# Kernel tuning notes

Hardware: AMD Instinct MI355X
Metric: run time of the kernel (lower is better)

The kernel has to match this reference:

```python
import jax, jax.numpy as jnp
import numpy as np

B, S, T = 16, 128, 128
E, H, D = 512, 512, 1024      # emb, encoder hidden, decoder hidden
VIN, VOUT = 10000, 10000


def setup_inputs() -> dict:
    key = jax.random.key(0)
    ks = iter(jax.random.split(key, 32))
    def w(shape, s=0.02):
        return jax.random.normal(next(ks), shape, jnp.float32) * s
    return {
        "x": jax.random.randint(next(ks), (B, S), 0, VIN),
        "gs_output": jax.random.randint(next(ks), (B, T), 0, VOUT),
        "in_emb": w((VIN, E)),
        "out_emb": w((VOUT, E)),
        "enc_wih0": w((2, 4 * H, E)), "enc_whh0": w((2, 4 * H, H)), "enc_b0": w((2, 4 * H)),
        "enc_wih1": w((2, 4 * H, 2 * H)), "enc_whh1": w((2, 4 * H, H)), "enc_b1": w((2, 4 * H)),
        "dec_wih0": w((4 * D, 2 * H + E)), "dec_whh0": w((4 * D, D)), "dec_b0": w((4 * D,)),
        "dec_wih1": w((4 * D, D)), "dec_whh1": w((4 * D, D)), "dec_b1": w((4 * D,)),
        "attn_w": w((D, 2 * H + D)), "attn_b": w((D,)),
        "attn_v": jax.random.uniform(next(ks), (D,), jnp.float32),
        "out_w": w((VOUT, D)), "out_b": w((VOUT,)),
    }


def _lstm_cell(x, h, c, wih, whh, b):
    # PyTorch gate order: i, f, g, o
    g = x @ wih.T + h @ whh.T + b
    i, f, gg, o = jnp.split(g, 4, axis=-1)
    c = jax.nn.sigmoid(f) * c + jax.nn.sigmoid(i) * jnp.tanh(gg)
    h = jax.nn.sigmoid(o) * jnp.tanh(c)
    return h, c


def _lstm_scan(xs, wih, whh, b, reverse=False):
    # xs: [T, B, in] time-major; returns hidden states [T, B, H]
    Bn, Hh = xs.shape[1], whh.shape[1]
    z = jnp.zeros((Bn, Hh), xs.dtype)
    def step(carry, x):
        h, c = _lstm_cell(x, carry[0], carry[1], wih, whh, b)
        return (h, c), h
    _, hs = jax.lax.scan(step, (z, z), xs, reverse=reverse)
    return hs


def reference(x, gs_output, in_emb, out_emb,
              enc_wih0, enc_whh0, enc_b0, enc_wih1, enc_whh1, enc_b1,
              dec_wih0, dec_whh0, dec_b0, dec_wih1, dec_whh1, dec_b1,
              attn_w, attn_b, attn_v, out_w, out_b):
    # padding_idx=0 rows are zero (matches nn.Embedding(padding_idx=0))
    in_emb = in_emb.at[0].set(0.0)
    out_emb = out_emb.at[0].set(0.0)
    Bn, Sn = x.shape

    # ---- bidirectional 2-layer encoder (eval mode, dropout off) ----
    xs = in_emb[x].transpose(1, 0, 2)  # [S, B, E]
    l0 = jnp.concatenate([
        _lstm_scan(xs, enc_wih0[0], enc_whh0[0], enc_b0[0]),
        _lstm_scan(xs, enc_wih0[1], enc_whh0[1], enc_b0[1], reverse=True)], -1)
    enc = jnp.concatenate([
        _lstm_scan(l0, enc_wih1[0], enc_whh1[0], enc_b1[0]),
        _lstm_scan(l0, enc_wih1[1], enc_whh1[1], enc_b1[1], reverse=True)], -1)
    enc_out = enc.transpose(1, 0, 2)  # [B, S, 2H]

    dec_layers = ((dec_wih0, dec_whh0, dec_b0), (dec_wih1, dec_whh1, dec_b1))

    def dec_step(h, c, inp):
        hs, cs = [], []
        for l, (wih, whh, b) in enumerate(dec_layers):
            nh, nc = _lstm_cell(inp, h[l], c[l], wih, whh, b)
            hs.append(nh); cs.append(nc); inp = nh
        return jnp.stack(hs), jnp.stack(cs), inp

    # torch primes decoder_hidden with one zero-input step from zero state
    h = jnp.zeros((2, Bn, D), jnp.float32)
    c = jnp.zeros((2, Bn, D), jnp.float32)
    h, c, _ = dec_step(h, c, jnp.zeros((Bn, 2 * H + E), jnp.float32))

    gs_emb = out_emb[gs_output].transpose(1, 0, 2)  # [T, B, E]

    def step(carry, emb_t):
        h, c, last_emb = carry
        q = c[-1]  # torch uses decoder_hidden[-1][-1] = last-layer CELL state
        qrep = jnp.broadcast_to(q[:, None, :], (Bn, Sn, D))
        energy = jnp.tanh(jnp.einsum('bsk,dk->bsd', jnp.concatenate([qrep, enc_out], -1), attn_w) + attn_b)
        a = jax.nn.softmax(energy @ attn_v, axis=1)           # [B, S]
        weighted = jnp.einsum('bs,bsh->bh', a, enc_out)       # [B, 2H]
        h2, c2, top = dec_step(h, c, jnp.concatenate([weighted, last_emb], -1))
        logits = top @ out_w.T + out_b                        # [B, Vout]
        return (h2, c2, emb_t), logits

    init = (h, c, jnp.zeros((Bn, E), jnp.float32))
    _, outs = jax.lax.scan(step, init, gs_emb)                # [T, B, Vout]
    return outs.transpose(1, 0, 2)                            # [B, T, Vout]
```

## Files before the change

### kernel.cpp

```cpp
#include <hip/hip_runtime.h>

#define BB 16
#define SS 128
#define TT 128
#define EE 512
#define HH 512
#define DD 1024
#define VO 10000

typedef _Float16 half4_t __attribute__((ext_vector_type(4)));
typedef _Float16 half8_t __attribute__((ext_vector_type(8)));

#define FMA4(A, W, X)              \
  A = fmaf((W).x, (X).x, A);       \
  A = fmaf((W).y, (X).y, A);       \
  A = fmaf((W).z, (X).z, A);       \
  A = fmaf((W).w, (X).w, A)

__device__ __forceinline__ float4 h2f4(half4_t h) {
  return make_float4((float)h[0], (float)h[1], (float)h[2], (float)h[3]);
}

__device__ __forceinline__ float wred(float s) {
#pragma unroll
  for (int off = 32; off >= 1; off >>= 1) s += __shfl_xor(s, off, 64);
  return s;
}
__device__ __forceinline__ float sigm(float x) { return 1.f / (1.f + expf(-x)); }

__device__ __forceinline__ void stv(float* p, float v) {
  __hip_atomic_store(p, v, __ATOMIC_RELAXED, __HIP_MEMORY_SCOPE_AGENT);
}

__device__ __forceinline__ void gbar2(unsigned* bar, int lb, int nblk, unsigned target) {
  asm volatile("s_waitcnt vmcnt(0) lgkmcnt(0)" ::: "memory");
  __syncthreads();
  if (threadIdx.x == 0)
    __hip_atomic_store(bar + lb * 16, target, __ATOMIC_RELAXED, __HIP_MEMORY_SCOPE_AGENT);
  if (lb == 0) {
    for (int i = threadIdx.x; i < nblk; i += blockDim.x)
      while (__hip_atomic_load(bar + i * 16, __ATOMIC_RELAXED, __HIP_MEMORY_SCOPE_AGENT) <
             target)
        __builtin_amdgcn_s_sleep(1);
    __syncthreads();
    if (threadIdx.x == 0)
      __hip_atomic_store(bar + 8192, target, __ATOMIC_RELAXED, __HIP_MEMORY_SCOPE_AGENT);
  }
  if (threadIdx.x == 0)
    while (__hip_atomic_load(bar + 8192, __ATOMIC_RELAXED, __HIP_MEMORY_SCOPE_AGENT) <
           target)
      __builtin_amdgcn_s_sleep(1);
  __syncthreads();
}

__global__ void f2h_k(const float* __restrict__ src, _Float16* __restrict__ dst, int n8) {
  const int i = blockIdx.x * blockDim.x + threadIdx.x;
  if (i < n8) {
    const float4 a = *(const float4*)&src[i * 8];
    const float4 b = *(const float4*)&src[i * 8 + 4];
    half8_t h;
    h[0] = a.x; h[1] = a.y; h[2] = a.z; h[3] = a.w;
    h[4] = b.x; h[5] = b.y; h[6] = b.z; h[7] = b.w;
    *(half8_t*)&dst[i * 8] = h;
  }
}

__global__ void gather_k(const int* __restrict__ idx, const float* __restrict__ emb,
                         float* __restrict__ out, int Sn) {
  const int s = blockIdx.x, b = blockIdx.y, tid = threadIdx.x;
  const int id = idx[b * Sn + s];
  float4 v = make_float4(0.f, 0.f, 0.f, 0.f);
  if (id != 0) v = ((const float4*)(emb + (size_t)id * EE))[tid];
  ((float4*)(out + ((size_t)s * BB + b) * EE))[tid] = v;
}

template <int K>
__global__ void gemv16b_k(const float* __restrict__ X, int ldx,
                          const float* __restrict__ W, int ldw,
                          float* __restrict__ G, int M, size_t wz, size_t gz) {
  const int lane = threadIdx.x & 63;
  const int n = blockIdx.x * 4 + (threadIdx.x >> 6);
  const int mg = blockIdx.y;
  const int z = blockIdx.z;
  const float* Xr = X + (size_t)mg * 16 * ldx;
  const float* Wn = W + (size_t)z * wz + (size_t)n * ldw;
  float acc[16];
#pragma unroll
  for (int j = 0; j < 16; ++j) acc[j] = 0.f;
#pragma unroll
  for (int it = 0; it < K / 256; ++it) {
    const int k = it * 256 + lane * 4;
    const float4 w4 = *(const float4*)&Wn[k];
#pragma unroll
    for (int j = 0; j < 16; ++j) {
      const float4 xv = *(const float4*)&Xr[(size_t)j * ldx + k];
      FMA4(acc[j], w4, xv);
    }
  }
#pragma unroll
  for (int j = 0; j < 16; ++j) acc[j] = wred(acc[j]);
  float sel = 0.f;
#pragma unroll
  for (int j = 0; j < 16; ++j)
    if (lane == j) sel = acc[j];
  if (lane < 16) G[(size_t)z * gz + (size_t)n * M + mg * 16 + lane] = sel;
}

__global__ __launch_bounds__(512, 4) void enc_mega7_k(
    const float* __restrict__ gx, const float* __restrict__ whh,
    const float* __restrict__ bias, float* __restrict__ h_all,
    float* __restrict__ seq, int seq_ts, int seq_bs, unsigned* __restrict__ barbase) {
  const int tid = threadIdx.x, lane = tid & 63, lw = tid >> 6;
  const int dir = blockIdx.x >> 7;
  const int lb = blockIdx.x & 127;
  const int w2 = lb * 8 + lw;
  const int d = w2 >> 1, bq = w2 & 1;
  unsigned* bar = barbase + dir * 16384;

  __shared__ float hs[16][512];

  float wr[4][8];
  const float* wsrc = whh + (size_t)dir * (4 * HH * HH);
#pragma unroll
  for (int g = 0; g < 4; ++g)
#pragma unroll
    for (int j = 0; j < 8; ++j)
      wr[g][j] = wsrc[(size_t)(g * HH + d) * HH + j * 64 + lane];
  float bv[4];
#pragma unroll
  for (int g = 0; g < 4; ++g) bv[g] = bias[dir * 4 * HH + g * HH + d];
  const float* gxz = gx + (size_t)dir * ((size_t)4 * HH * 2048);
  float creg = 0.f;
  unsigned bt = 0;

  for (int t = 0; t < SS; ++t) {
    const int idx = dir ? (SS - 1 - t) : t;
    const float* hp = h_all + ((size_t)t * 2 + dir) * (BB * HH);
    for (int i = tid; i < BB * HH / 4; i += 512)
      *(float4*)&((float*)hs)[i * 4] = *(const float4*)&hp[i * 4];
    __syncthreads();
    float acc[4][8];
#pragma unroll
    for (int g = 0; g < 4; ++g)
#pragma unroll
      for (int j = 0; j < 8; ++j) acc[g][j] = 0.f;
#pragma unroll
    for (int kb = 0; kb < 8; ++kb) {
      const int k = kb * 64 + lane;
#pragma unroll
      for (int j = 0; j < 8; ++j) {
        const float xv = hs[bq * 8 + j][k];
#pragma unroll
        for (int g = 0; g < 4; ++g) acc[g][j] = fmaf(wr[g][kb], xv, acc[g][j]);
      }
    }
#pragma unroll
    for (int g = 0; g < 4; ++g)
#pragma unroll
      for (int j = 0; j < 8; ++j) acc[g][j] = wred(acc[g][j]);
    float s0 = 0.f, s1 = 0.f, s2 = 0.f, s3 = 0.f;
#pragma unroll
    for (int j = 0; j < 8; ++j)
      if (lane == j) { s0 = acc[0][j]; s1 = acc[1][j]; s2 = acc[2][j]; s3 = acc[3][j]; }
    if (lane < 8) {
      const int b = bq * 8 + lane;
      const int m = idx * 16 + b;
      const float gi = sigm(s0 + bv[0] + gxz[(size_t)(0 * HH + d) * 2048 + m]);
      const float gf = sigm(s1 + bv[1] + gxz[(size_t)(1 * HH + d) * 2048 + m]);
      const float gg = tanhf(s2 + bv[2] + gxz[(size_t)(2 * HH + d) * 2048 + m]);
      const float go = sigm(s3 + bv[3] + gxz[(size_t)(3 * HH + d) * 2048 + m]);
      const float cn = gf * creg + gi * gg;
      creg = cn;
      const float hv = go * tanhf(cn);
      stv(h_all + ((size_t)(t + 1) * 2 + dir) * (BB * HH) + b * HH + d, hv);
      seq[(size_t)idx * seq_ts + (size_t)b * seq_bs + dir * HH + d] = hv;
    }
    gbar2(bar, lb, 128, ++bt);
  }
}

__global__ __launch_bounds__(1024, 4) void dec_mega7h_k(
    const float* __restrict__ gs_emb, const float* __restrict__ encWe,
    const float* __restrict__ enc_out, const _Float16* __restrict__ aw16,
    const float* __restrict__ attn_b, const float* __restrict__ attn_v,
    const _Float16* __restrict__ w16i0, const _Float16* __restrict__ w16h0,
    const float* __restrict__ b0, const _Float16* __restrict__ w16i1,
    const _Float16* __restrict__ w16h1, const float* __restrict__ b1,
    const float* __restrict__ zeros, float* __restrict__ h0_all,
    float* __restrict__ h1_all, float* __restrict__ c1_all, float* __restrict__ wtd_all,
    float* __restrict__ qW_all, float* __restrict__ scores_all,
    unsigned* __restrict__ bar) {
  const int tid = threadIdx.x, lane = tid & 63, lw = tid >> 6;
  const int blk = blockIdx.x;
  const int w = blk * 16 + lw;
  const int d = w >> 2, bq = w & 3;
  const int b_att = blk >> 4, shard = blk & 15;

  __shared__ float xch[4][4][16];
  __shared__ float sco[SS];
  __shared__ float sred[16][64];

  const _Float16* w0i0 = w16i0 + (size_t)(0 * DD + d) * 1536;
  const _Float16* w0i1 = w16i0 + (size_t)(1 * DD + d) * 1536;
  const _Float16* w0i2 = w16i0 + (size_t)(2 * DD + d) * 1536;
  const _Float16* w0i3 = w16i0 + (size_t)(3 * DD + d) * 1536;
  const _Float16* w0h0 = w16h0 + (size_t)(0 * DD + d) * 1024;
  const _Float16* w0h1 = w16h0 + (size_t)(1 * DD + d) * 1024;
  const _Float16* w0h2 = w16h0 + (size_t)(2 * DD + d) * 1024;
  const _Float16* w0h3 = w16h0 + (size_t)(3 * DD + d) * 1024;
  const _Float16* w1i0 = w16i1 + (size_t)(0 * DD + d) * 1024;
  const _Float16* w1i1 = w16i1 + (size_t)(1 * DD + d) * 1024;
  const _Float16* w1i2 = w16i1 + (size_t)(2 * DD + d) * 1024;
  const _Float16* w1i3 = w16i1 + (size_t)(3 * DD + d) * 1024;
  const _Float16* w1h0 = w16h1 + (size_t)(0 * DD + d) * 1024;
  const _Float16* w1h1 = w16h1 + (size_t)(1 * DD + d) * 1024;
  const _Float16* w1h2 = w16h1 + (size_t)(2 * DD + d) * 1024;
  const _Float16* w1h3 = w16h1 + (size_t)(3 * DD + d) * 1024;
  float bv0[4], bv1[4];
#pragma unroll
  for (int g = 0; g < 4; ++g) { bv0[g] = b0[g * DD + d]; bv1[g] = b1[g * DD + d]; }
  const float abv = attn_b[d];
  float c0 = 0.f, c1 = 0.f;
  unsigned bt = 0;

  if (lw == ((d & 3) << 2) && lane < 16) {
  }
  if (bq == 0 && lane < 16) {
  }
  if (bq == 0 && lane < 16) {
    const float cn = sigm(bv0[0]) * tanhf(bv0[2]);
    c0 = cn;
    stv(h0_all + lane * DD + d, sigm(bv0[3]) * tanhf(cn));
  }
  gbar2(bar, blk, 256, ++bt);
  {
    float acc[4][4];
#pragma unroll
    for (int g = 0; g < 4; ++g)
#pragma unroll
      for (int j = 0; j < 4; ++j) acc[g][j] = 0.f;
#pragma unroll
    for (int it = 0; it < 4; ++it) {
      const int k = it * 256 + lane * 4;
      const float4 q0 = h2f4(*(const half4_t*)&w1i0[k]);
      const float4 q1 = h2f4(*(const half4_t*)&w1i1[k]);
      const float4 q2 = h2f4(*(const half4_t*)&w1i2[k]);
      const float4 q3 = h2f4(*(const half4_t*)&w1i3[k]);
#pragma unroll
      for (int j = 0; j < 4; ++j) {
        const float4 xv = *(const float4*)&h0_all[(bq * 4 + j) * DD + k];
        FMA4(acc[0][j], q0, xv);
        FMA4(acc[1][j], q1, xv);
        FMA4(acc[2][j], q2, xv);
        FMA4(acc[3][j], q3, xv);
      }
    }
#pragma unroll
    for (int g = 0; g < 4; ++g)
#pragma unroll
      for (int j = 0; j < 4; ++j) acc[g][j] = wred(acc[g][j]);
    float s[4] = {0.f, 0.f, 0.f, 0.f};
#pragma unroll
    for (int j = 0; j < 4; ++j)
      if (lane == j) { s[0] = acc[0][j]; s[1] = acc[1][j]; s[2] = acc[2][j]; s[3] = acc[3][j]; }
    if (lane < 4) {
      const int b = bq * 4 + lane;
      const float cn = sigm(s[0] + bv1[0]) * tanhf(s[2] + bv1[2]);
      c1 = cn;
      stv(c1_all + b * DD + d, cn);
      stv(h1_all + b * DD + d, sigm(s[3] + bv1[3]) * tanhf(cn));
    }
  }
  gbar2(bar, blk, 256, ++bt);

  for (int t = 0; t < TT; ++t) {
    {
      const float* cb = c1_all + (size_t)t * (BB * DD);
      float qa[4] = {0.f, 0.f, 0.f, 0.f};
#pragma unroll
      for (int it = 0; it < 4; ++it) {
        const int k = it * 256 + lane * 4;
        const float4 w4 = h2f4(*(const half4_t*)&aw16[(size_t)d * 2048 + k]);
#pragma unroll
        for (int j = 0; j < 4; ++j) {
          const float4 xv = *(const float4*)&cb[(bq * 4 + j) * DD + k];
          FMA4(qa[j], w4, xv);
        }
      }
#pragma unroll
      for (int j = 0; j < 4; ++j) qa[j] = wred(qa[j]);
      float sel = 0.f;
#pragma unroll
      for (int j = 0; j < 4; ++j)
        if (lane == j) sel = qa[j];
      if (lane < 4)
        stv(qW_all + (size_t)t * (BB * DD) + (bq * 4 + lane) * DD + d, sel + abv);
    }
    gbar2(bar, blk, 256, ++bt);
    if (lw < 8) {
      const int s = shard * 8 + lw;
      const float* ew = encWe + ((size_t)(b_att * SS + s)) * DD;
      const float* qb = qW_all + (size_t)t * (BB * DD) + b_att * DD;
      float a = 0.f;
#pragma unroll
      for (int it = 0; it < 4; ++it) {
        const int k = it * 256 + lane * 4;
        const float4 e4 = *(const float4*)&ew[k];
        const float4 q4 = *(const float4*)&qb[k];
        const float4 v4 = *(const float4*)&attn_v[k];
        a += v4.x * tanhf(q4.x + e4.x) + v4.y * tanhf(q4.y + e4.y) +
             v4.z * tanhf(q4.z + e4.z) + v4.w * tanhf(q4.w + e4.w);
      }
      a = wred(a);
      if (lane == 0) stv(scores_all + (size_t)t * (BB * SS) + b_att * SS + s, a);
    }
    gbar2(bar, blk, 256, ++bt);
    {
      if (tid < SS) sco[tid] = scores_all[(size_t)t * (BB * SS) + b_att * SS + tid];
      __syncthreads();
      float m = -1e30f;
      for (int s = 0; s < SS; ++s) m = fmaxf(m, sco[s]);
      __syncthreads();
      if (tid < SS) sco[tid] = expf(sco[tid] - m);
      __syncthreads();
      float sum = 0.f;
      for (int s = 0; s < SS; ++s) sum += sco[s];
      const float inv = 1.f / sum;
      float p = 0.f;
#pragma unroll
      for (int i = 0; i < 8; ++i) {
        const int s = lw * 8 + i;
        p += sco[s] * enc_out[((size_t)(b_att * SS + s)) * DD + shard * 64 + lane];
      }
      sred[lw][lane] = p;
      __syncthreads();
      if (lw == 0) {
        float a2 = 0.f;
#pragma unroll
        for (int i = 0; i < 16; ++i) a2 += sred[i][lane];
        stv(wtd_all + (size_t)t * (BB * DD) + b_att * DD + shard * 64 + lane, a2 * inv);
      }
    }
    gbar2(bar, blk, 256, ++bt);
    {
      const float* xw = wtd_all + (size_t)t * (BB * DD);
      const float* em = t ? gs_emb + (size_t)(t - 1) * (BB * EE) : zeros;
      const float* hp = h0_all + (size_t)t * (BB * DD);
      float acc[4][4];
#pragma unroll
      for (int g = 0; g < 4; ++g)
#pragma unroll
        for (int j = 0; j < 4; ++j) acc[g][j] = 0.f;
#pragma unroll
      for (int it = 0; it < 4; ++it) {
        const int k = it * 256 + lane * 4;
        const float4 q0 = h2f4(*(const half4_t*)&w0i0[k]);
        const float4 q1 = h2f4(*(const half4_t*)&w0i1[k]);
        const float4 q2 = h2f4(*(const half4_t*)&w0i2[k]);
        const float4 q3 = h2f4(*(const half4_t*)&w0i3[k]);
#pragma unroll
        for (int j = 0; j < 4; ++j) {
          const float4 xv = *(const float4*)&xw[(bq * 4 + j) * DD + k];
          FMA4(acc[0][j], q0, xv);
          FMA4(acc[1][j], q1, xv);
          FMA4(acc[2][j], q2, xv);
          FMA4(acc[3][j], q3, xv);
        }
      }
#pragma unroll
      for (int it = 4; it < 6; ++it) {
        const int k = it * 256 + lane * 4;
        const float4 q0 = h2f4(*(const half4_t*)&w0i0[k]);
        const float4 q1 = h2f4(*(const half4_t*)&w0i1[k]);
        const float4 q2 = h2f4(*(const half4_t*)&w0i2[k]);
        const float4 q3 = h2f4(*(const half4_t*)&w0i3[k]);
#pragma unroll
        for (int j = 0; j < 4; ++j) {
          const float4 xv = *(const float4*)&em[(bq * 4 + j) * EE + (k - 1024)];
          FMA4(acc[0][j], q0, xv);
          FMA4(acc[1][j], q1, xv);
          FMA4(acc[2][j], q2, xv);
          FMA4(acc[3][j], q3, xv);
        }
      }
#pragma unroll
      for (int it = 0; it < 4; ++it) {
        const int k = it * 256 + lane * 4;
        const float4 q0 = h2f4(*(const half4_t*)&w0h0[k]);
        const float4 q1 = h2f4(*(const half4_t*)&w0h1[k]);
        const float4 q2 = h2f4(*(const half4_t*)&w0h2[k]);
        const float4 q3 = h2f4(*(const half4_t*)&w0h3[k]);
#pragma unroll
        for (int j = 0; j < 4; ++j) {
          const float4 xv = *(const float4*)&hp[(bq * 4 + j) * DD + k];
          FMA4(acc[0][j], q0, xv);
          FMA4(acc[1][j], q1, xv);
          FMA4(acc[2][j], q2, xv);
          FMA4(acc[3][j], q3, xv);
        }
      }
#pragma unroll
      for (int g = 0; g < 4; ++g)
#pragma unroll
        for (int j = 0; j < 4; ++j) acc[g][j] = wred(acc[g][j]);
      float s[4] = {0.f, 0.f, 0.f, 0.f};
#pragma unroll
      for (int j = 0; j < 4; ++j)
        if (lane == j) { s[0] = acc[0][j]; s[1] = acc[1][j]; s[2] = acc[2][j]; s[3] = acc[3][j]; }
      if (lane < 4) {
        const int b = bq * 4 + lane;
        const float cn = sigm(s[1] + bv0[1]) * c0 + sigm(s[0] + bv0[0]) * tanhf(s[2] + bv0[2]);
        c0 = cn;
        stv(h0_all + (size_t)(t + 1) * (BB * DD) + b * DD + d,
            sigm(s[3] + bv0[3]) * tanhf(cn));
      }
    }
    gbar2(bar, blk, 256, ++bt);
    {
      const float* h0 = h0_all + (size_t)(t + 1) * (BB * DD);
      const float* h1p = h1_all + (size_t)t * (BB * DD);
      float acc[4][4];
#pragma unroll
      for (int g = 0; g < 4; ++g)
#pragma unroll
        for (int j = 0; j < 4; ++j) acc[g][j] = 0.f;
#pragma unroll
      for (int it = 0; it < 4; ++it) {
        const int k = it * 256 + lane * 4;
        const float4 q0 = h2f4(*(const half4_t*)&w1i0[k]);
        const float4 q1 = h2f4(*(const half4_t*)&w1i1[k]);
        const float4 q2 = h2f4(*(const half4_t*)&w1i2[k]);
        const float4 q3 = h2f4(*(const half4_t*)&w1i3[k]);
#pragma unroll
        for (int j = 0; j < 4; ++j) {
          const float4 xv = *(const float4*)&h0[(bq * 4 + j) * DD + k];
          FMA4(acc[0][j], q0, xv);
          FMA4(acc[1][j], q1, xv);
          FMA4(acc[2][j], q2, xv);
          FMA4(acc[3][j], q3, xv);
        }
      }
#pragma unroll
      for (int it = 0; it < 4; ++it) {
        const int k = it * 256 + lane * 4;
        const float4 q0 = h2f4(*(const half4_t*)&w1h0[k]);
        const float4 q1 = h2f4(*(const half4_t*)&w1h1[k]);
        const float4 q2 = h2f4(*(const half4_t*)&w1h2[k]);
        const float4 q3 = h2f4(*(const half4_t*)&w1h3[k]);
#pragma unroll
        for (int j = 0; j < 4; ++j) {
          const float4 xv = *(const float4*)&h1p[(bq * 4 + j) * DD + k];
          FMA4(acc[0][j], q0, xv);
          FMA4(acc[1][j], q1, xv);
          FMA4(acc[2][j], q2, xv);
          FMA4(acc[3][j], q3, xv);
        }
      }
#pragma unroll
      for (int g = 0; g < 4; ++g)
#pragma unroll
        for (int j = 0; j < 4; ++j) acc[g][j] = wred(acc[g][j]);
      float s[4] = {0.f, 0.f, 0.f, 0.f};
#pragma unroll
      for (int j = 0; j < 4; ++j)
        if (lane == j) { s[0] = acc[0][j]; s[1] = acc[1][j]; s[2] = acc[2][j]; s[3] = acc[3][j]; }
      if (lane < 4) {
        const int b = bq * 4 + lane;
        const float cn = sigm(s[1] + bv1[1]) * c1 + sigm(s[0] + bv1[0]) * tanhf(s[2] + bv1[2]);
        c1 = cn;
        stv(c1_all + (size_t)(t + 1) * (BB * DD) + b * DD + d, cn);
        stv(h1_all + (size_t)(t + 1) * (BB * DD) + b * DD + d,
            sigm(s[3] + bv1[3]) * tanhf(cn));
      }
    }
    gbar2(bar, blk, 256, ++bt);
  }
}

__global__ __launch_bounds__(512) void encwe2_k(const float* __restrict__ enc_out,
                                                const float* __restrict__ attn_w,
                                                float* __restrict__ encWe) {
  const int tid = threadIdx.x, lane = tid & 63, lw = tid >> 6;
  const int mg = blockIdx.x;
  const int nq = blockIdx.y;
  __shared__ float xsl[16][1024];
  for (int i = tid; i < 16 * 1024 / 4; i += 512)
    *(float4*)&((float*)xsl)[i * 4] =
        *(const float4*)&enc_out[(size_t)mg * 16 * 1024 + i * 4];
  __syncthreads();
#pragma unroll 1
  for (int nn = 0; nn < 8; ++nn) {
    const int n = nq * 64 + lw * 8 + nn;
    float acc[16];
#pragma unroll
    for (int j = 0; j < 16; ++j) acc[j] = 0.f;
#pragma unroll
    for (int it = 0; it < 4; ++it) {
      const int k = it * 256 + lane * 4;
      const float4 w4 = *(const float4*)&attn_w[(size_t)n * 2048 + 1024 + k];
#pragma unroll
      for (int j = 0; j < 16; ++j) {
        const float4 xv = *(const float4*)&xsl[j][k];
        FMA4(acc[j], w4, xv);
      }
    }
#pragma unroll
    for (int j = 0; j < 16; ++j) acc[j] = wred(acc[j]);
    float sel = 0.f;
#pragma unroll
    for (int j = 0; j < 16; ++j)
      if (lane == j) sel = acc[j];
    if (lane < 16) encWe[((size_t)mg * 16 + lane) * 1024 + n] = sel;
  }
}

__global__ __launch_bounds__(1024, 4) void logits2_k(const float* __restrict__ h1all,
                                                     const float* __restrict__ out_w,
                                                     const float* __restrict__ out_b,
                                                     float* __restrict__ out) {
  const int tid = threadIdx.x, lane = tid & 63, lw = tid >> 6;
  const int t = blockIdx.x;
  const int oq = blockIdx.y;
  __shared__ float hs[16][1024];
  const float* h1 = h1all + (size_t)t * (BB * DD);
  for (int i = tid; i < BB * DD / 4; i += 1024)
    *(float4*)&((float*)hs)[i * 4] = *(const float4*)&h1[i * 4];
  __syncthreads();
  const int obase = oq * 80 + lw * 5;
#pragma unroll
  for (int p = 0; p < 3; ++p) {
    const int nr = (p < 2) ? 2 : 1;
    const int o0 = obase + p * 2;
    float accA[16], accB[16];
#pragma unroll
    for (int b = 0; b < 16; ++b) { accA[b] = 0.f; accB[b] = 0.f; }
    const float* wr0 = out_w + (size_t)o0 * DD;
    const float* wr1 = wr0 + DD;
#pragma unroll
    for (int it = 0; it < 4; ++it) {
      const int k = it * 256 + lane * 4;
      const float4 wa = *(const float4*)&wr0[k];
      float4 wb = make_float4(0.f, 0.f, 0.f, 0.f);
      if (nr == 2) wb = *(const float4*)&wr1[k];
#pragma unroll
      for (int b = 0; b < 16; ++b) {
        const float4 xv = *(const float4*)&hs[b][k];
        FMA4(accA[b], wa, xv);
        if (nr == 2) { FMA4(accB[b], wb, xv); }
      }
    }
#pragma unroll
    for (int b = 0; b < 16; ++b) {
      accA[b] = wred(accA[b]);
      if (nr == 2) accB[b] = wred(accB[b]);
    }
    float sA = 0.f, sB = 0.f;
#pragma unroll
    for (int b = 0; b < 16; ++b)
      if (lane == b) { sA = accA[b]; sB = accB[b]; }
    if (lane < 16) {
      out[(size_t)lane * TT * VO + (size_t)t * VO + o0] = sA + out_b[o0];
      if (nr == 2) out[(size_t)lane * TT * VO + (size_t)t * VO + o0 + 1] = sB + out_b[o0 + 1];
    }
  }
}

extern "C" void kernel_launch(void* const* d_in, const int* in_sizes, int n_in,
                              void* d_out, int out_size, void* d_ws, size_t ws_size,
                              hipStream_t stream) {
  const int* x = (const int*)d_in[0];
  const int* gs = (const int*)d_in[1];
  const float* in_emb = (const float*)d_in[2];
  const float* out_emb = (const float*)d_in[3];
  const float* ewih0 = (const float*)d_in[4];
  const float* ewhh0 = (const float*)d_in[5];
  const float* eb0 = (const float*)d_in[6];
  const float* ewih1 = (const float*)d_in[7];
  const float* ewhh1 = (const float*)d_in[8];
  const float* eb1 = (const float*)d_in[9];
  const float* dwih0 = (const float*)d_in[10];
  const float* dwhh0 = (const float*)d_in[11];
  const float* db0 = (const float*)d_in[12];
  const float* dwih1 = (const float*)d_in[13];
  const float* dwhh1 = (const float*)d_in[14];
  const float* db1 = (const float*)d_in[15];
  const float* attn_w = (const float*)d_in[16];
  const float* attn_b = (const float*)d_in[17];
  const float* attn_v = (const float*)d_in[18];
  const float* out_w = (const float*)d_in[19];
  const float* out_b = (const float*)d_in[20];
  float* out = (float*)d_out;

  float* ws = (float*)d_ws;
  size_t off = 0;
  auto alloc = [&](size_t n) { float* p = ws + off; off += n; return p; };
  unsigned* bar = (unsigned*)alloc(5 * 16384);
  float* zeros = alloc(BB * DD);
  float* ehA = alloc((size_t)(SS + 1) * 2 * BB * HH);
  float* ehB = alloc(2 * BB * HH);
  const size_t state_n = off;
  alloc((size_t)SS * 2 * BB * HH);
  _Float16* w16i0 = (_Float16*)alloc(4096 * 1536 / 2);
  _Float16* w16h0 = (_Float16*)alloc(4096 * 1024 / 2);
  _Float16* w16i1 = (_Float16*)alloc(4096 * 1024 / 2);
  _Float16* w16h1 = (_Float16*)alloc(4096 * 1024 / 2);
  _Float16* aw16 = (_Float16*)alloc(1024 * 2048 / 2);
  float* h0_all = alloc((size_t)(TT + 1) * BB * DD);
  float* h1_all = alloc((size_t)(TT + 1) * BB * DD);
  float* c1_all = alloc((size_t)(TT + 1) * BB * DD);
  float* wtd_all = alloc((size_t)TT * BB * DD);
  float* qW_all = alloc((size_t)TT * BB * DD);
  float* scores_all = alloc((size_t)TT * BB * SS);
  float* xs_emb = alloc((size_t)SS * BB * EE);
  float* gs_emb = alloc((size_t)TT * BB * EE);
  float* l0 = alloc((size_t)SS * BB * (2 * HH));
  float* enc_out = alloc((size_t)BB * SS * (2 * HH));
  float* encWe = alloc((size_t)BB * SS * DD);
  float* gxA = alloc(2ull * 2048ull * 2048ull);
  (void)ws_size; (void)in_sizes; (void)n_in; (void)out_size;

  hipMemsetAsync(d_ws, 0, state_n * sizeof(float), stream);

  f2h_k<<<(4096 * 1536 / 8 + 255) / 256, 256, 0, stream>>>(dwih0, w16i0, 4096 * 1536 / 8);
  f2h_k<<<(4096 * 1024 / 8 + 255) / 256, 256, 0, stream>>>(dwhh0, w16h0, 4096 * 1024 / 8);
  f2h_k<<<(4096 * 1024 / 8 + 255) / 256, 256, 0, stream>>>(dwih1, w16i1, 4096 * 1024 / 8);
  f2h_k<<<(4096 * 1024 / 8 + 255) / 256, 256, 0, stream>>>(dwhh1, w16h1, 4096 * 1024 / 8);
  f2h_k<<<(1024 * 2048 / 8 + 255) / 256, 256, 0, stream>>>(attn_w, aw16, 1024 * 2048 / 8);

  gather_k<<<dim3(SS, BB), 128, 0, stream>>>(x, in_emb, xs_emb, SS);
  gather_k<<<dim3(TT, BB), 128, 0, stream>>>(gs, out_emb, gs_emb, TT);

  gemv16b_k<EE><<<dim3(512, 128, 2), 256, 0, stream>>>(
      xs_emb, EE, ewih0, EE, gxA, 2048, (size_t)4 * HH * EE, 2048ull * 2048ull);
  enc_mega7_k<<<256, 512, 0, stream>>>(gxA, ewhh0, eb0, ehA, l0, BB * 2 * HH, 2 * HH, bar);
  gemv16b_k<2 * HH><<<dim3(512, 128, 2), 256, 0, stream>>>(
      l0, 2 * HH, ewih1, 2 * HH, gxA, 2048, (size_t)4 * HH * 2 * HH, 2048ull * 2048ull);
  enc_mega7_k<<<256, 512, 0, stream>>>(gxA, ewhh1, eb1, ehB, enc_out, 2 * HH, SS * 2 * HH,
                                       bar + 2 * 16384);
  encwe2_k<<<dim3(128, 16), 512, 0, stream>>>(enc_out, attn_w, encWe);

  dec_mega7h_k<<<256, 1024, 0, stream>>>(gs_emb, encWe, enc_out, aw16, attn_b, attn_v,
                                         w16i0, w16h0, db0, w16i1, w16h1, db1, zeros,
                                         h0_all, h1_all, c1_all, wtd_all, qW_all,
                                         scores_all, bar + 4 * 16384);

  logits2_k<<<dim3(TT, 125), 1024, 0, stream>>>(h1_all + BB * DD, out_w, out_b, out);
}
```

Baseline: 15.10 ms.

## Widen decoder megakernel to 512 blocks, use fp16 logits weights, loop gemv over batches

```diff
diff --git a/kernel.cpp b/kernel.cpp
--- a/kernel.cpp
+++ b/kernel.cpp
@@ -75,35 +75,37 @@
 }
 
 template <int K>
-__global__ void gemv16b_k(const float* __restrict__ X, int ldx,
+__global__ void gemv16c_k(const float* __restrict__ X, int ldx,
                           const float* __restrict__ W, int ldw,
                           float* __restrict__ G, int M, size_t wz, size_t gz) {
   const int lane = threadIdx.x & 63;
   const int n = blockIdx.x * 4 + (threadIdx.x >> 6);
-  const int mg = blockIdx.y;
-  const int z = blockIdx.z;
-  const float* Xr = X + (size_t)mg * 16 * ldx;
+  const int z = blockIdx.y;
   const float* Wn = W + (size_t)z * wz + (size_t)n * ldw;
-  float acc[16];
-#pragma unroll
-  for (int j = 0; j < 16; ++j) acc[j] = 0.f;
-#pragma unroll
-  for (int it = 0; it < K / 256; ++it) {
-    const int k = it * 256 + lane * 4;
-    const float4 w4 = *(const float4*)&Wn[k];
-#pragma unroll
-    for (int j = 0; j < 16; ++j) {
-      const float4 xv = *(const float4*)&Xr[(size_t)j * ldx + k];
-      FMA4(acc[j], w4, xv);
-    }
-  }
-#pragma unroll
-  for (int j = 0; j < 16; ++j) acc[j] = wred(acc[j]);
-  float sel = 0.f;
-#pragma unroll
-  for (int j = 0; j < 16; ++j)
-    if (lane == j) sel = acc[j];
-  if (lane < 16) G[(size_t)z * gz + (size_t)n * M + mg * 16 + lane] = sel;
+#pragma unroll 1
+  for (int mg = 0; mg < M / 16; ++mg) {
+    const float* Xr = X + (size_t)mg * 16 * ldx;
+    float acc[16];
+#pragma unroll
+    for (int j = 0; j < 16; ++j) acc[j] = 0.f;
+#pragma unroll
+    for (int it = 0; it < K / 256; ++it) {
+      const int k = it * 256 + lane * 4;
+      const float4 w4 = *(const float4*)&Wn[k];
+#pragma unroll
+      for (int j = 0; j < 16; ++j) {
+        const float4 xv = *(const float4*)&Xr[(size_t)j * ldx + k];
+        FMA4(acc[j], w4, xv);
+      }
+    }
+#pragma unroll
+    for (int j = 0; j < 16; ++j) acc[j] = wred(acc[j]);
+    float sel = 0.f;
+#pragma unroll
+    for (int j = 0; j < 16; ++j)
+      if (lane == j) sel = acc[j];
+    if (lane < 16) G[(size_t)z * gz + (size_t)n * M + mg * 16 + lane] = sel;
+  }
 }
 
 __global__ __launch_bounds__(512, 4) void enc_mega7_k(
@@ -179,7 +181,7 @@
   }
 }
 
-__global__ __launch_bounds__(1024, 4) void dec_mega7h_k(
+__global__ __launch_bounds__(1024, 8) void dec_megaA_k(
     const float* __restrict__ gs_emb, const float* __restrict__ encWe,
     const float* __restrict__ enc_out, const _Float16* __restrict__ aw16,
     const float* __restrict__ attn_b, const float* __restrict__ attn_v,
@@ -192,13 +194,13 @@
     unsigned* __restrict__ bar) {
   const int tid = threadIdx.x, lane = tid & 63, lw = tid >> 6;
   const int blk = blockIdx.x;
-  const int w = blk * 16 + lw;
-  const int d = w >> 2, bq = w & 3;
-  const int b_att = blk >> 4, shard = blk & 15;
-
-  __shared__ float xch[4][4][16];
+  const int dl = lw >> 3;
+  const int d = blk * 2 + dl;
+  const int bp = lw & 7;
+  const int b_att = blk >> 5, shard = blk & 31;
+
   __shared__ float sco[SS];
-  __shared__ float sred[16][64];
+  __shared__ float sred[32][33];
 
   const _Float16* w0i0 = w16i0 + (size_t)(0 * DD + d) * 1536;
   const _Float16* w0i1 = w16i0 + (size_t)(1 * DD + d) * 1536;
@@ -223,22 +225,16 @@
   float c0 = 0.f, c1 = 0.f;
   unsigned bt = 0;
 
-  if (lw == ((d & 3) << 2) && lane < 16) {
-  }
-  if (bq == 0 && lane < 16) {
-  }
-  if (bq == 0 && lane < 16) {
+  {
     const float cn = sigm(bv0[0]) * tanhf(bv0[2]);
     c0 = cn;
-    stv(h0_all + lane * DD + d, sigm(bv0[3]) * tanhf(cn));
-  }
-  gbar2(bar, blk, 256, ++bt);
+    if (lane < 2) stv(h0_all + (bp * 2 + lane) * DD + d, sigm(bv0[3]) * tanhf(cn));
+  }
+  gbar2(bar, blk, 512, ++bt);
   {
-    float acc[4][4];
-#pragma unroll
-    for (int g = 0; g < 4; ++g)
-#pragma unroll
-      for (int j = 0; j < 4; ++j) acc[g][j] = 0.f;
+    float acc[4][2];
+#pragma unroll
+    for (int g = 0; g < 4; ++g) { acc[g][0] = 0.f; acc[g][1] = 0.f; }
 #pragma unroll
     for (int it = 0; it < 4; ++it) {
       const int k = it * 256 + lane * 4;
@@ -247,8 +243,8 @@
       const float4 q2 = h2f4(*(const half4_t*)&w1i2[k]);
       const float4 q3 = h2f4(*(const half4_t*)&w1i3[k]);
 #pragma unroll
-      for (int j = 0; j < 4; ++j) {
-        const float4 xv = *(const float4*)&h0_all[(bq * 4 + j) * DD + k];
+      for (int j = 0; j < 2; ++j) {
+        const float4 xv = *(const float4*)&h0_all[(bp * 2 + j) * DD + k];
         FMA4(acc[0][j], q0, xv);
         FMA4(acc[1][j], q1, xv);
         FMA4(acc[2][j], q2, xv);
@@ -256,49 +252,46 @@
       }
     }
 #pragma unroll
-    for (int g = 0; g < 4; ++g)
-#pragma unroll
-      for (int j = 0; j < 4; ++j) acc[g][j] = wred(acc[g][j]);
+    for (int g = 0; g < 4; ++g) { acc[g][0] = wred(acc[g][0]); acc[g][1] = wred(acc[g][1]); }
     float s[4] = {0.f, 0.f, 0.f, 0.f};
 #pragma unroll
-    for (int j = 0; j < 4; ++j)
+    for (int j = 0; j < 2; ++j)
       if (lane == j) { s[0] = acc[0][j]; s[1] = acc[1][j]; s[2] = acc[2][j]; s[3] = acc[3][j]; }
-    if (lane < 4) {
-      const int b = bq * 4 + lane;
+    if (lane < 2) {
+      const int b = bp * 2 + lane;
       const float cn = sigm(s[0] + bv1[0]) * tanhf(s[2] + bv1[2]);
       c1 = cn;
       stv(c1_all + b * DD + d, cn);
       stv(h1_all + b * DD + d, sigm(s[3] + bv1[3]) * tanhf(cn));
     }
   }
-  gbar2(bar, blk, 256, ++bt);
+  gbar2(bar, blk, 512, ++bt);
 
   for (int t = 0; t < TT; ++t) {
     {
       const float* cb = c1_all + (size_t)t * (BB * DD);
-      float qa[4] = {0.f, 0.f, 0.f, 0.f};
+      float qa[2] = {0.f, 0.f};
 #pragma unroll
       for (int it = 0; it < 4; ++it) {
         const int k = it * 256 + lane * 4;
         const float4 w4 = h2f4(*(const half4_t*)&aw16[(size_t)d * 2048 + k]);
 #pragma unroll
-        for (int j = 0; j < 4; ++j) {
-          const float4 xv = *(const float4*)&cb[(bq * 4 + j) * DD + k];
+        for (int j = 0; j < 2; ++j) {
+          const float4 xv = *(const float4*)&cb[(bp * 2 + j) * DD + k];
           FMA4(qa[j], w4, xv);
         }
       }
-#pragma unroll
-      for (int j = 0; j < 4; ++j) qa[j] = wred(qa[j]);
+      qa[0] = wred(qa[0]);
+      qa[1] = wred(qa[1]);
       float sel = 0.f;
-#pragma unroll
-      for (int j = 0; j < 4; ++j)
-        if (lane == j) sel = qa[j];
-      if (lane < 4)
-        stv(qW_all + (size_t)t * (BB * DD) + (bq * 4 + lane) * DD + d, sel + abv);
-    }
-    gbar2(bar, blk, 256, ++bt);
-    if (lw < 8) {
-      const int s = shard * 8 + lw;
+      if (lane == 0) sel = qa[0];
+      if (lane == 1) sel = qa[1];
+      if (lane < 2)
+        stv(qW_all + (size_t)t * (BB * DD) + (bp * 2 + lane) * DD + d, sel + abv);
+    }
+    gbar2(bar, blk, 512, ++bt);
+    if (lw < 4) {
+      const int s = shard * 4 + lw;
       const float* ew = encWe + ((size_t)(b_att * SS + s)) * DD;
       const float* qb = qW_all + (size_t)t * (BB * DD) + b_att * DD;
       float a = 0.f;
@@ -314,7 +307,7 @@
       a = wred(a);
       if (lane == 0) stv(scores_all + (size_t)t * (BB * SS) + b_att * SS + s, a);
     }
-    gbar2(bar, blk, 256, ++bt);
+    gbar2(bar, blk, 512, ++bt);
     {
       if (tid < SS) sco[tid] = scores_all[(size_t)t * (BB * SS) + b_att * SS + tid];
       __syncthreads();
@@ -326,31 +319,30 @@
       float sum = 0.f;
       for (int s = 0; s < SS; ++s) sum += sco[s];
       const float inv = 1.f / sum;
+      const int col = tid & 31, sg = tid >> 5;
       float p = 0.f;
 #pragma unroll
-      for (int i = 0; i < 8; ++i) {
-        const int s = lw * 8 + i;
-        p += sco[s] * enc_out[((size_t)(b_att * SS + s)) * DD + shard * 64 + lane];
-      }
-      sred[lw][lane] = p;
+      for (int i = 0; i < 4; ++i) {
+        const int s = sg * 4 + i;
+        p += sco[s] * enc_out[((size_t)(b_att * SS + s)) * DD + shard * 32 + col];
+      }
+      sred[sg][col] = p;
       __syncthreads();
-      if (lw == 0) {
+      if (tid < 32) {
         float a2 = 0.f;
 #pragma unroll
-        for (int i = 0; i < 16; ++i) a2 += sred[i][lane];
-        stv(wtd_all + (size_t)t * (BB * DD) + b_att * DD + shard * 64 + lane, a2 * inv);
-      }
-    }
-    gbar2(bar, blk, 256, ++bt);
+        for (int i = 0; i < 32; ++i) a2 += sred[i][tid];
+        stv(wtd_all + (size_t)t * (BB * DD) + b_att * DD + shard * 32 + tid, a2 * inv);
+      }
+    }
+    gbar2(bar, blk, 512, ++bt);
     {
       const float* xw = wtd_all + (size_t)t * (BB * DD);
       const float* em = t ? gs_emb + (size_t)(t - 1) * (BB * EE) : zeros;
       const float* hp = h0_all + (size_t)t * (BB * DD);
-      float acc[4][4];
-#pragma unroll
-      for (int g = 0; g < 4; ++g)
-#pragma unroll
-        for (int j = 0; j < 4; ++j) acc[g][j] = 0.f;
+      float acc[4][2];
+#pragma unroll
+      for (int g = 0; g < 4; ++g) { acc[g][0] = 0.f; acc[g][1] = 0.f; }
 #pragma unroll
       for (int it = 0; it < 4; ++it) {
         const int k = it * 256 + lane * 4;
@@ -359,8 +351,8 @@
         const float4 q2 = h2f4(*(const half4_t*)&w0i2[k]);
         const float4 q3 = h2f4(*(const half4_t*)&w0i3[k]);
 #pragma unroll
-        for (int j = 0; j < 4; ++j) {
-          const float4 xv = *(const float4*)&xw[(bq * 4 + j) * DD + k];
+        for (int j = 0; j < 2; ++j) {
+          const float4 xv = *(const float4*)&xw[(bp * 2 + j) * DD + k];
           FMA4(acc[0][j], q0, xv);
           FMA4(acc[1][j], q1, xv);
           FMA4(acc[2][j], q2, xv);
@@ -375,8 +367,8 @@
         const float4 q2 = h2f4(*(const half4_t*)&w0i2[k]);
         const float4 q3 = h2f4(*(const half4_t*)&w0i3[k]);
 #pragma unroll
-        for (int j = 0; j < 4; ++j) {
-          const float4 xv = *(const float4*)&em[(bq * 4 + j) * EE + (k - 1024)];
+        for (int j = 0; j < 2; ++j) {
+          const float4 xv = *(const float4*)&em[(bp * 2 + j) * EE + (k - 1024)];
           FMA4(acc[0][j], q0, xv);
           FMA4(acc[1][j], q1, xv);
           FMA4(acc[2][j], q2, xv);
@@ -391,8 +383,8 @@
         const float4 q2 = h2f4(*(const half4_t*)&w0h2[k]);
         const float4 q3 = h2f4(*(const half4_t*)&w0h3[k]);
 #pragma unroll
-        for (int j = 0; j < 4; ++j) {
-          const float4 xv = *(const float4*)&hp[(bq * 4 + j) * DD + k];
+        for (int j = 0; j < 2; ++j) {
+          const float4 xv = *(const float4*)&hp[(bp * 2 + j) * DD + k];
           FMA4(acc[0][j], q0, xv);
           FMA4(acc[1][j], q1, xv);
           FMA4(acc[2][j], q2, xv);
@@ -400,30 +392,26 @@
         }
       }
 #pragma unroll
-      for (int g = 0; g < 4; ++g)
-#pragma unroll
-        for (int j = 0; j < 4; ++j) acc[g][j] = wred(acc[g][j]);
+      for (int g = 0; g < 4; ++g) { acc[g][0] = wred(acc[g][0]); acc[g][1] = wred(acc[g][1]); }
       float s[4] = {0.f, 0.f, 0.f, 0.f};
 #pragma unroll
-      for (int j = 0; j < 4; ++j)
+      for (int j = 0; j < 2; ++j)
         if (lane == j) { s[0] = acc[0][j]; s[1] = acc[1][j]; s[2] = acc[2][j]; s[3] = acc[3][j]; }
-      if (lane < 4) {
-        const int b = bq * 4 + lane;
+      if (lane < 2) {
+        const int b = bp * 2 + lane;
         const float cn = sigm(s[1] + bv0[1]) * c0 + sigm(s[0] + bv0[0]) * tanhf(s[2] + bv0[2]);
         c0 = cn;
         stv(h0_all + (size_t)(t + 1) * (BB * DD) + b * DD + d,
             sigm(s[3] + bv0[3]) * tanhf(cn));
       }
     }
-    gbar2(bar, blk, 256, ++bt);
+    gbar2(bar, blk, 512, ++bt);
     {
       const float* h0 = h0_all + (size_t)(t + 1) * (BB * DD);
       const float* h1p = h1_all + (size_t)t * (BB * DD);
-      float acc[4][4];
-#pragma unroll
-      for (int g = 0; g < 4; ++g)
-#pragma unroll
-        for (int j = 0; j < 4; ++j) acc[g][j] = 0.f;
+      float acc[4][2];
+#pragma unroll
+      for (int g = 0; g < 4; ++g) { acc[g][0] = 0.f; acc[g][1] = 0.f; }
 #pragma unroll
       for (int it = 0; it < 4; ++it) {
         const int k = it * 256 + lane * 4;
@@ -432,8 +420,8 @@
         const float4 q2 = h2f4(*(const half4_t*)&w1i2[k]);
         const float4 q3 = h2f4(*(const half4_t*)&w1i3[k]);
 #pragma unroll
-        for (int j = 0; j < 4; ++j) {
-          const float4 xv = *(const float4*)&h0[(bq * 4 + j) * DD + k];
+        for (int j = 0; j < 2; ++j) {
+          const float4 xv = *(const float4*)&h0[(bp * 2 + j) * DD + k];
           FMA4(acc[0][j], q0, xv);
           FMA4(acc[1][j], q1, xv);
           FMA4(acc[2][j], q2, xv);
@@ -448,8 +436,8 @@
         const float4 q2 = h2f4(*(const half4_t*)&w1h2[k]);
         const float4 q3 = h2f4(*(const half4_t*)&w1h3[k]);
 #pragma unroll
-        for (int j = 0; j < 4; ++j) {
-          const float4 xv = *(const float4*)&h1p[(bq * 4 + j) * DD + k];
+        for (int j = 0; j < 2; ++j) {
+          const float4 xv = *(const float4*)&h1p[(bp * 2 + j) * DD + k];
           FMA4(acc[0][j], q0, xv);
           FMA4(acc[1][j], q1, xv);
           FMA4(acc[2][j], q2, xv);
@@ -457,15 +445,13 @@
         }
       }
 #pragma unroll
-      for (int g = 0; g < 4; ++g)
-#pragma unroll
-        for (int j = 0; j < 4; ++j) acc[g][j] = wred(acc[g][j]);
+      for (int g = 0; g < 4; ++g) { acc[g][0] = wred(acc[g][0]); acc[g][1] = wred(acc[g][1]); }
       float s[4] = {0.f, 0.f, 0.f, 0.f};
 #pragma unroll
-      for (int j = 0; j < 4; ++j)
+      for (int j = 0; j < 2; ++j)
         if (lane == j) { s[0] = acc[0][j]; s[1] = acc[1][j]; s[2] = acc[2][j]; s[3] = acc[3][j]; }
-      if (lane < 4) {
-        const int b = bq * 4 + lane;
+      if (lane < 2) {
+        const int b = bp * 2 + lane;
         const float cn = sigm(s[1] + bv1[1]) * c1 + sigm(s[0] + bv1[0]) * tanhf(s[2] + bv1[2]);
         c1 = cn;
         stv(c1_all + (size_t)(t + 1) * (BB * DD) + b * DD + d, cn);
@@ -473,7 +459,7 @@
             sigm(s[3] + bv1[3]) * tanhf(cn));
       }
     }
-    gbar2(bar, blk, 256, ++bt);
+    gbar2(bar, blk, 512, ++bt);
   }
 }
 
@@ -514,10 +500,10 @@
   }
 }
 
-__global__ __launch_bounds__(1024, 4) void logits2_k(const float* __restrict__ h1all,
-                                                     const float* __restrict__ out_w,
-                                                     const float* __restrict__ out_b,
-                                                     float* __restrict__ out) {
+__global__ __launch_bounds__(1024, 2) void logits2h_k(const float* __restrict__ h1all,
+                                                      const _Float16* __restrict__ ow16,
+                                                      const float* __restrict__ out_b,
+                                                      float* __restrict__ out) {
   const int tid = threadIdx.x, lane = tid & 63, lw = tid >> 6;
   const int t = blockIdx.x;
   const int oq = blockIdx.y;
@@ -534,14 +520,14 @@
     float accA[16], accB[16];
 #pragma unroll
     for (int b = 0; b < 16; ++b) { accA[b] = 0.f; accB[b] = 0.f; }
-    const float* wr0 = out_w + (size_t)o0 * DD;
-    const float* wr1 = wr0 + DD;
+    const _Float16* wr0 = ow16 + (size_t)o0 * DD;
+    const _Float16* wr1 = wr0 + DD;
 #pragma unroll
     for (int it = 0; it < 4; ++it) {
       const int k = it * 256 + lane * 4;
-      const float4 wa = *(const float4*)&wr0[k];
+      const float4 wa = h2f4(*(const half4_t*)&wr0[k]);
       float4 wb = make_float4(0.f, 0.f, 0.f, 0.f);
-      if (nr == 2) wb = *(const float4*)&wr1[k];
+      if (nr == 2) wb = h2f4(*(const half4_t*)&wr1[k]);
 #pragma unroll
       for (int b = 0; b < 16; ++b) {
         const float4 xv = *(const float4*)&hs[b][k];
@@ -605,6 +591,7 @@
   _Float16* w16i1 = (_Float16*)alloc(4096 * 1024 / 2);
   _Float16* w16h1 = (_Float16*)alloc(4096 * 1024 / 2);
   _Float16* aw16 = (_Float16*)alloc(1024 * 2048 / 2);
+  _Float16* ow16 = (_Float16*)alloc((size_t)VO * DD / 2);
   float* h0_all = alloc((size_t)(TT + 1) * BB * DD);
   float* h1_all = alloc((size_t)(TT + 1) * BB * DD);
   float* c1_all = alloc((size_t)(TT + 1) * BB * DD);
@@ -626,23 +613,24 @@
   f2h_k<<<(4096 * 1024 / 8 + 255) / 256, 256, 0, stream>>>(dwih1, w16i1, 4096 * 1024 / 8);
   f2h_k<<<(4096 * 1024 / 8 + 255) / 256, 256, 0, stream>>>(dwhh1, w16h1, 4096 * 1024 / 8);
   f2h_k<<<(1024 * 2048 / 8 + 255) / 256, 256, 0, stream>>>(attn_w, aw16, 1024 * 2048 / 8);
+  f2h_k<<<(VO * DD / 8 + 255) / 256, 256, 0, stream>>>(out_w, ow16, VO * DD / 8);
 
   gather_k<<<dim3(SS, BB), 128, 0, stream>>>(x, in_emb, xs_emb, SS);
   gather_k<<<dim3(TT, BB), 128, 0, stream>>>(gs, out_emb, gs_emb, TT);
 
-  gemv16b_k<EE><<<dim3(512, 128, 2), 256, 0, stream>>>(
+  gemv16c_k<EE><<<dim3(512, 2), 256, 0, stream>>>(
       xs_emb, EE, ewih0, EE, gxA, 2048, (size_t)4 * HH * EE, 2048ull * 2048ull);
   enc_mega7_k<<<256, 512, 0, stream>>>(gxA, ewhh0, eb0, ehA, l0, BB * 2 * HH, 2 * HH, bar);
-  gemv16b_k<2 * HH><<<dim3(512, 128, 2), 256, 0, stream>>>(
+  gemv16c_k<2 * HH><<<dim3(512, 2), 256, 0, stream>>>(
       l0, 2 * HH, ewih1, 2 * HH, gxA, 2048, (size_t)4 * HH * 2 * HH, 2048ull * 2048ull);
   enc_mega7_k<<<256, 512, 0, stream>>>(gxA, ewhh1, eb1, ehB, enc_out, 2 * HH, SS * 2 * HH,
                                        bar + 2 * 16384);
   encwe2_k<<<dim3(128, 16), 512, 0, stream>>>(enc_out, attn_w, encWe);
 
-  dec_mega7h_k<<<256, 1024, 0, stream>>>(gs_emb, encWe, enc_out, aw16, attn_b, attn_v,
-                                         w16i0, w16h0, db0, w16i1, w16h1, db1, zeros,
-                                         h0_all, h1_all, c1_all, wtd_all, qW_all,
-                                         scores_all, bar + 4 * 16384);
-
-  logits2_k<<<dim3(TT, 125), 1024, 0, stream>>>(h1_all + BB * DD, out_w, out_b, out);
-}
+  dec_megaA_k<<<512, 1024, 0, stream>>>(gs_emb, encWe, enc_out, aw16, attn_b, attn_v,
+                                        w16i0, w16h0, db0, w16i1, w16h1, db1, zeros,
+                                        h0_all, h1_all, c1_all, wtd_all, qW_all,
+                                        scores_all, bar + 4 * 16384);
+
+  logits2h_k<<<dim3(TT, 125), 1024, 0, stream>>>(h1_all + BB * DD, ow16, out_b, out);
+}
```

Result: slower. 33.26 ms (+120.3%).

## Use fp16 output weights in logits, loop row groups in input GEMV

Applied to the files above, without the earlier changes.

```diff
diff --git a/kernel.cpp b/kernel.cpp
--- a/kernel.cpp
+++ b/kernel.cpp
@@ -75,35 +75,37 @@
 }
 
 template <int K>
-__global__ void gemv16b_k(const float* __restrict__ X, int ldx,
+__global__ void gemv16c_k(const float* __restrict__ X, int ldx,
                           const float* __restrict__ W, int ldw,
                           float* __restrict__ G, int M, size_t wz, size_t gz) {
   const int lane = threadIdx.x & 63;
   const int n = blockIdx.x * 4 + (threadIdx.x >> 6);
-  const int mg = blockIdx.y;
-  const int z = blockIdx.z;
-  const float* Xr = X + (size_t)mg * 16 * ldx;
+  const int z = blockIdx.y;
   const float* Wn = W + (size_t)z * wz + (size_t)n * ldw;
-  float acc[16];
-#pragma unroll
-  for (int j = 0; j < 16; ++j) acc[j] = 0.f;
-#pragma unroll
-  for (int it = 0; it < K / 256; ++it) {
-    const int k = it * 256 + lane * 4;
-    const float4 w4 = *(const float4*)&Wn[k];
-#pragma unroll
-    for (int j = 0; j < 16; ++j) {
-      const float4 xv = *(const float4*)&Xr[(size_t)j * ldx + k];
-      FMA4(acc[j], w4, xv);
-    }
-  }
-#pragma unroll
-  for (int j = 0; j < 16; ++j) acc[j] = wred(acc[j]);
-  float sel = 0.f;
-#pragma unroll
-  for (int j = 0; j < 16; ++j)
-    if (lane == j) sel = acc[j];
-  if (lane < 16) G[(size_t)z * gz + (size_t)n * M + mg * 16 + lane] = sel;
+#pragma unroll 1
+  for (int mg = 0; mg < M / 16; ++mg) {
+    const float* Xr = X + (size_t)mg * 16 * ldx;
+    float acc[16];
+#pragma unroll
+    for (int j = 0; j < 16; ++j) acc[j] = 0.f;
+#pragma unroll
+    for (int it = 0; it < K / 256; ++it) {
+      const int k = it * 256 + lane * 4;
+      const float4 w4 = *(const float4*)&Wn[k];
+#pragma unroll
+      for (int j = 0; j < 16; ++j) {
+        const float4 xv = *(const float4*)&Xr[(size_t)j * ldx + k];
+        FMA4(acc[j], w4, xv);
+      }
+    }
+#pragma unroll
+    for (int j = 0; j < 16; ++j) acc[j] = wred(acc[j]);
+    float sel = 0.f;
+#pragma unroll
+    for (int j = 0; j < 16; ++j)
+      if (lane == j) sel = acc[j];
+    if (lane < 16) G[(size_t)z * gz + (size_t)n * M + mg * 16 + lane] = sel;
+  }
 }
 
 __global__ __launch_bounds__(512, 4) void enc_mega7_k(
@@ -223,14 +225,11 @@
   float c0 = 0.f, c1 = 0.f;
   unsigned bt = 0;
 
-  if (lw == ((d & 3) << 2) && lane < 16) {
-  }
-  if (bq == 0 && lane < 16) {
-  }
-  if (bq == 0 && lane < 16) {
+  {
     const float cn = sigm(bv0[0]) * tanhf(bv0[2]);
     c0 = cn;
-    stv(h0_all + lane * DD + d, sigm(bv0[3]) * tanhf(cn));
+    if (bq == 0 && lane < 16)
+      stv(h0_all + lane * DD + d, sigm(bv0[3]) * tanhf(cn));
   }
   gbar2(bar, blk, 256, ++bt);
   {
@@ -514,10 +513,10 @@
   }
 }
 
-__global__ __launch_bounds__(1024, 4) void logits2_k(const float* __restrict__ h1all,
-                                                     const float* __restrict__ out_w,
-                                                     const float* __restrict__ out_b,
-                                                     float* __restrict__ out) {
+__global__ __launch_bounds__(1024, 2) void logits2h_k(const float* __restrict__ h1all,
+                                                      const _Float16* __restrict__ ow16,
+                                                      const float* __restrict__ out_b,
+                                                      float* __restrict__ out) {
   const int tid = threadIdx.x, lane = tid & 63, lw = tid >> 6;
   const int t = blockIdx.x;
   const int oq = blockIdx.y;
@@ -534,14 +533,14 @@
     float accA[16], accB[16];
 #pragma unroll
     for (int b = 0; b < 16; ++b) { accA[b] = 0.f; accB[b] = 0.f; }
-    const float* wr0 = out_w + (size_t)o0 * DD;
-    const float* wr1 = wr0 + DD;
+    const _Float16* wr0 = ow16 + (size_t)o0 * DD;
+    const _Float16* wr1 = wr0 + DD;
 #pragma unroll
     for (int it = 0; it < 4; ++it) {
       const int k = it * 256 + lane * 4;
-      const float4 wa = *(const float4*)&wr0[k];
+      const float4 wa = h2f4(*(const half4_t*)&wr0[k]);
       float4 wb = make_float4(0.f, 0.f, 0.f, 0.f);
-      if (nr == 2) wb = *(const float4*)&wr1[k];
+      if (nr == 2) wb = h2f4(*(const half4_t*)&wr1[k]);
 #pragma unroll
       for (int b = 0; b < 16; ++b) {
         const float4 xv = *(const float4*)&hs[b][k];
@@ -605,6 +604,7 @@
   _Float16* w16i1 = (_Float16*)alloc(4096 * 1024 / 2);
   _Float16* w16h1 = (_Float16*)alloc(4096 * 1024 / 2);
   _Float16* aw16 = (_Float16*)alloc(1024 * 2048 / 2);
+  _Float16* ow16 = (_Float16*)alloc((size_t)VO * DD / 2);
   float* h0_all = alloc((size_t)(TT + 1) * BB * DD);
   float* h1_all = alloc((size_t)(TT + 1) * BB * DD);
   float* c1_all = alloc((size_t)(TT + 1) * BB * DD);
@@ -626,14 +626,15 @@
   f2h_k<<<(4096 * 1024 / 8 + 255) / 256, 256, 0, stream>>>(dwih1, w16i1, 4096 * 1024 / 8);
   f2h_k<<<(4096 * 1024 / 8 + 255) / 256, 256, 0, stream>>>(dwhh1, w16h1, 4096 * 1024 / 8);
   f2h_k<<<(1024 * 2048 / 8 + 255) / 256, 256, 0, stream>>>(attn_w, aw16, 1024 * 2048 / 8);
+  f2h_k<<<(VO * DD / 8 + 255) / 256, 256, 0, stream>>>(out_w, ow16, VO * DD / 8);
 
   gather_k<<<dim3(SS, BB), 128, 0, stream>>>(x, in_emb, xs_emb, SS);
   gather_k<<<dim3(TT, BB), 128, 0, stream>>>(gs, out_emb, gs_emb, TT);
 
-  gemv16b_k<EE><<<dim3(512, 128, 2), 256, 0, stream>>>(
+  gemv16c_k<EE><<<dim3(512, 2), 256, 0, stream>>>(
       xs_emb, EE, ewih0, EE, gxA, 2048, (size_t)4 * HH * EE, 2048ull * 2048ull);
   enc_mega7_k<<<256, 512, 0, stream>>>(gxA, ewhh0, eb0, ehA, l0, BB * 2 * HH, 2 * HH, bar);
-  gemv16b_k<2 * HH><<<dim3(512, 128, 2), 256, 0, stream>>>(
+  gemv16c_k<2 * HH><<<dim3(512, 2), 256, 0, stream>>>(
       l0, 2 * HH, ewih1, 2 * HH, gxA, 2048, (size_t)4 * HH * 2 * HH, 2048ull * 2048ull);
   enc_mega7_k<<<256, 512, 0, stream>>>(gxA, ewhh1, eb1, ehB, enc_out, 2 * HH, SS * 2 * HH,
                                        bar + 2 * 16384);
@@ -644,5 +645,5 @@
                                          h0_all, h1_all, c1_all, wtd_all, qW_all,
                                          scores_all, bar + 4 * 16384);
 
-  logits2_k<<<dim3(TT, 125), 1024, 0, stream>>>(h1_all + BB * DD, out_w, out_b, out);
-}
+  logits2h_k<<<dim3(TT, 125), 1024, 0, stream>>>(h1_all + BB * DD, ow16, out_b, out);
+}
```

Measured after the change: 15.43 ms. 2.2% more time.
